# Optimization experiments

Measured on AMD Instinct MI355X. Metric: run time of the kernel, lower is better.

## Reference

```python
import jax, jax.numpy as jnp
import numpy as np

B, T, D, L, H = 8, 1024, 768, 8, 12
BLOCK_SIZE = 4
HD = D // H


def setup_inputs() -> dict:
    key = jax.random.key(0)
    ks = jax.random.split(key, 10)
    sd = 0.02
    return {
        "x_init": jax.random.normal(ks[0], (B, T, D), jnp.float32),
        "attn_proj_w": jax.random.normal(ks[1], (L, D), jnp.float32) * sd,
        "mlp_proj_w": jax.random.normal(ks[2], (L, D), jnp.float32) * sd,
        "Wqkv": jax.random.normal(ks[3], (L, D, 3 * D), jnp.float32) * sd,
        "Wo": jax.random.normal(ks[4], (L, D, D), jnp.float32) * sd,
        "Wm1": jax.random.normal(ks[5], (L, D, 4 * D), jnp.float32) * sd,
        "Wm2": jax.random.normal(ks[6], (L, 4 * D, D), jnp.float32) * sd,
        "attn_scale": 1.0 + jax.random.normal(ks[7], (L, D), jnp.float32) * sd,
        "mlp_scale": 1.0 + jax.random.normal(ks[8], (L, D), jnp.float32) * sd,
        "ln_s": jnp.ones((L,), jnp.float32),
    }


def _rms_norm(x):
    # F.rms_norm with eps=None -> eps = finfo(dtype).eps
    eps = jnp.finfo(x.dtype).eps
    return x * jax.lax.rsqrt(jnp.mean(x * x, axis=-1, keepdims=True) + eps)


def _aggregate(V, q):
    # V: [n, B, T, D]; scalar-query depth attention (keys RMS-normed, values raw)
    K = _rms_norm(V)
    logits = jnp.einsum('d,nbtd->nbt', q, K)
    w = jax.nn.softmax(logits, axis=0)
    return jnp.einsum('nbt,nbtd->btd', w, V)


def _mha(x, wqkv, wo):
    # causal multi-head self-attention
    b, t, d = x.shape
    qkv = x @ wqkv                                   # [b, t, 3D]
    q, k, v = jnp.split(qkv, 3, axis=-1)
    q = q.reshape(b, t, H, HD)
    k = k.reshape(b, t, H, HD)
    v = v.reshape(b, t, H, HD)
    scores = jnp.einsum('bqhd,bkhd->bhqk', q, k) / np.sqrt(HD).astype(np.float32)
    mask = jnp.tril(jnp.ones((t, t), bool))
    scores = jnp.where(mask[None, None], scores, jnp.asarray(-1e30, scores.dtype))
    attn = jax.nn.softmax(scores, axis=-1)
    out = jnp.einsum('bhqk,bkhd->bqhd', attn, v).reshape(b, t, d)
    return out @ wo


def reference(x_init, attn_proj_w, mlp_proj_w, Wqkv, Wo, Wm1, Wm2,
              attn_scale, mlp_scale, ln_s):
    boundary_every = max(1, BLOCK_SIZE // 2)
    hist = [x_init]          # committed block representations
    partial = x_init         # intra-block partial accumulator
    for l in range(L):
        s = ln_s[l]
        V = jnp.stack(hist + [partial], axis=0)          # [n_hist+1, B, T, D]
        h = _aggregate(V, attn_proj_w[l])
        if l % boundary_every == 0:
            hist.append(partial)
            partial = jnp.zeros_like(partial)
        attn_out = _mha(_rms_norm(h) * s, Wqkv[l], Wo[l])
        partial = partial + attn_scale[l][None, None, :] * attn_out
        V2 = jnp.stack(hist + [partial], axis=0)
        h = _aggregate(V2, mlp_proj_w[l])
        mlp_out = jax.nn.gelu((_rms_norm(h) * s) @ Wm1[l]) @ Wm2[l]
        partial = partial + mlp_scale[l][None, None, :] * mlp_out
    return partial
```

## Files before the change

### kernel.cpp

```cpp
#include <hip/hip_runtime.h>
#include <hip/hip_bf16.h>
#include <math.h>
#include <stdint.h>

#define D_MODEL 768
#define T_SEQ   1024
#define B_BATCH 8
#define NHEAD   12
#define HDIM    64
#define NLAYER  8

typedef unsigned short u16;
typedef __attribute__((ext_vector_type(8))) short bf16x8;
typedef __attribute__((ext_vector_type(4))) float f32x4;
typedef __attribute__((ext_vector_type(4))) uint32_t u32x4;

static constexpr size_t BTD  = (size_t)B_BATCH * T_SEQ * D_MODEL;
static constexpr int    ROWS = B_BATCH * T_SEQ;
static constexpr float  EPSF = 1.1920928955078125e-07f;


__device__ __forceinline__ u16 f2bf(float x) {
    __hip_bfloat16 h = __float2bfloat16(x);
    return __builtin_bit_cast(u16, h);
}
__device__ __forceinline__ float bf2f(u16 u) {
    __hip_bfloat16 h = __builtin_bit_cast(__hip_bfloat16, u);
    return __bfloat162float(h);
}
__device__ __forceinline__ void split_bf(float x, u16& hi, u16& lo) {
    hi = f2bf(x);
    lo = f2bf(x - bf2f(hi));
}
__device__ __forceinline__ uint32_t cvt_pk_bf16(float a, float b) {
    uint32_t r;
    asm("v_cvt_pk_bf16_f32 %0, %1, %2" : "=v"(r) : "v"(a), "v"(b));
    return r;
}
__device__ __forceinline__ f32x4 mfma16(bf16x8 a, bf16x8 b, f32x4 c) {
    return __builtin_amdgcn_mfma_f32_16x16x32_bf16(a, b, c, 0, 0, 0);
}

__device__ __forceinline__ void gl_lds16(const void* g, void* l) {
    auto gp = reinterpret_cast<const __attribute__((address_space(1))) char*>(
        reinterpret_cast<uintptr_t>(g));
    auto lp = reinterpret_cast<__attribute__((address_space(3))) char*>(
        static_cast<uint32_t>(reinterpret_cast<uintptr_t>(l)));
    __builtin_amdgcn_global_load_lds(gp, lp, 16, 0, 0);
}

__device__ __forceinline__ float block_reduce_sum(float v, float* sbuf) {
    #pragma unroll
    for (int off = 32; off > 0; off >>= 1) v += __shfl_down(v, off);
    __syncthreads();
    if ((threadIdx.x & 63) == 0) sbuf[threadIdx.x >> 6] = v;
    __syncthreads();
    return sbuf[0] + sbuf[1] + sbuf[2] + sbuf[3];
}

__device__ __forceinline__ float gelu_fast(float x) {
    float z = 0.7978845608028654f * (x + 0.044715f * x * x * x);
    float e = __expf(2.f * z);
    return x - x / (e + 1.f);
}

template<int N>
__global__ __launch_bounds__(256)
void agg_norm_kernel(const float* __restrict__ v0, const float* __restrict__ v1,
                     const float* __restrict__ v2, const float* __restrict__ v3,
                     const float* __restrict__ v4, const float* __restrict__ v5,
                     const float* __restrict__ q,  const float* __restrict__ lns,
                     u16* __restrict__ xh, u16* __restrict__ xl) {
    __shared__ float sbuf[4];
    const float* V[6] = {v0, v1, v2, v3, v4, v5};
    const size_t row = blockIdx.x;
    const int tid = threadIdx.x;

    float qv[3];
    #pragma unroll
    for (int j = 0; j < 3; ++j) qv[j] = q[tid + j * 256];

    float vv[N][3];
    float logits[N];
    #pragma unroll
    for (int i = 0; i < N; ++i) {
        const float* vr = V[i] + row * D_MODEL;
        float ssq = 0.f, qd = 0.f;
        #pragma unroll
        for (int j = 0; j < 3; ++j) {
            float x = vr[tid + j * 256];
            vv[i][j] = x;
            ssq = fmaf(x, x, ssq);
            qd  = fmaf(qv[j], x, qd);
        }
        float S  = block_reduce_sum(ssq, sbuf);
        float Qd = block_reduce_sum(qd,  sbuf);
        logits[i] = Qd * rsqrtf(S * (1.f / 768.f) + EPSF);
    }
    float mx = logits[0];
    #pragma unroll
    for (int i = 1; i < N; ++i) mx = fmaxf(mx, logits[i]);
    float w[N];
    float wsum = 0.f;
    #pragma unroll
    for (int i = 0; i < N; ++i) { w[i] = __expf(logits[i] - mx); wsum += w[i]; }
    float inv = 1.f / wsum;

    float outv[3] = {0.f, 0.f, 0.f};
    #pragma unroll
    for (int i = 0; i < N; ++i) {
        float wi = w[i] * inv;
        #pragma unroll
        for (int j = 0; j < 3; ++j) outv[j] = fmaf(wi, vv[i][j], outv[j]);
    }
    float ssq = 0.f;
    #pragma unroll
    for (int j = 0; j < 3; ++j) ssq = fmaf(outv[j], outv[j], ssq);
    float S2 = block_reduce_sum(ssq, sbuf);
    float scale = lns[0] * rsqrtf(S2 * (1.f / 768.f) + EPSF);
    #pragma unroll
    for (int j = 0; j < 3; ++j) {
        float x = outv[j] * scale;
        u16 hi, lo;
        split_bf(x, hi, lo);
        size_t idx = row * D_MODEL + tid + j * 256;
        xh[idx] = hi;
        xl[idx] = lo;
    }
}

__global__ __launch_bounds__(256)
void transpose_split(const float* __restrict__ W, u16* __restrict__ Th,
                     int K, int N) {
    __shared__ float t[32][33];
    const int bk = blockIdx.x * 32, bn = blockIdx.y * 32;
    const int r = threadIdx.x >> 3, c4 = (threadIdx.x & 7) * 4;
    float4 v = *(const float4*)&W[(size_t)(bk + r) * N + bn + c4];
    t[r][c4 + 0] = v.x; t[r][c4 + 1] = v.y; t[r][c4 + 2] = v.z; t[r][c4 + 3] = v.w;
    __syncthreads();
    u16 h[4];
    #pragma unroll
    for (int j = 0; j < 4; ++j) h[j] = f2bf(t[c4 + j][r]);
    size_t o = (size_t)(bn + r) * K + bk + c4;
    *(uint2*)&Th[o] = make_uint2((uint32_t)h[0] | ((uint32_t)h[1] << 16),
                                 (uint32_t)h[2] | ((uint32_t)h[3] << 16));
}

__global__ __launch_bounds__(256)
void vt_transpose(const u16* __restrict__ vh, u16* __restrict__ vth) {
    __shared__ u16 th[32][36];
    const int bh = blockIdx.z;
    const int t0 = blockIdx.x * 32, d0 = blockIdx.y * 32;
    const int r = threadIdx.x >> 3, c = (threadIdx.x & 7) * 4;
    const size_t ib = ((size_t)(bh << 10) + t0 + r) * 64 + d0 + c;
    *(uint2*)&th[r][c] = *(const uint2*)&vh[ib];
    __syncthreads();
    const size_t ob = ((size_t)(bh << 6) + d0 + r) * 1024 + t0 + c;
    u16 a0 = th[c + 0][r], a1 = th[c + 1][r], a2 = th[c + 2][r], a3 = th[c + 3][r];
    *(uint2*)&vth[ob] = make_uint2((uint32_t)a0 | ((uint32_t)a1 << 16),
                                   (uint32_t)a2 | ((uint32_t)a3 << 16));
}

template<int EPI, int BN, bool TWO>
__global__ __launch_bounds__(256)
void gemm_bf2(const u16* __restrict__ Ah, const u16* __restrict__ Al,
              const u16* __restrict__ Bh,
              float* __restrict__ Cf, u16* __restrict__ Ch,
              const float* __restrict__ scale, int M, int N, int K,
              u16* __restrict__ Qh, u16* __restrict__ Ql,
              u16* __restrict__ Kh, u16* __restrict__ Vh) {
    constexpr int NJ = BN / 32;
    constexpr int A_U16 = TWO ? 8192 : 4096;
    constexpr int BUF_U16 = A_U16 + BN * 32;
    __shared__ u16 smem[2 * BUF_U16];

    const int nwg = gridDim.x * gridDim.y;
    const int lin = blockIdx.y * gridDim.x + blockIdx.x;
    const int wg  = (lin & 7) * (nwg >> 3) + (lin >> 3);
    const int bm  = (wg / gridDim.x) << 7;
    const int bn  = (wg % gridDim.x) * BN;

    const int tid = threadIdx.x;
    const int w = tid >> 6, l = tid & 63;
    const int wr = w >> 1, wc = w & 1;

    const int grow = tid >> 2;
    const int gcol = (((tid & 3) ^ ((tid >> 3) & 3)) << 3);
    const size_t aoff0 = (size_t)(bm + grow) * K + gcol;
    const size_t boff0 = (size_t)(bn + grow) * K + gcol;
    const size_t s64 = (size_t)64 * K;
    char* sb0 = (char*)smem;
    char* sb1 = (char*)smem + 2 * BUF_U16;
    const uint32_t wq = (uint32_t)w << 10;

    auto stage = [&](char* sbuf, int k0) {
        gl_lds16(Ah + aoff0 + k0,       sbuf + 0    + wq);
        gl_lds16(Ah + aoff0 + s64 + k0, sbuf + 4096 + wq);
        if constexpr (TWO) {
            gl_lds16(Al + aoff0 + k0,       sbuf + 8192  + wq);
            gl_lds16(Al + aoff0 + s64 + k0, sbuf + 12288 + wq);
        }
        gl_lds16(Bh + boff0 + k0, sbuf + 2 * A_U16 + wq);
        if constexpr (BN == 128)
            gl_lds16(Bh + boff0 + s64 + k0, sbuf + 2 * A_U16 + 4096 + wq);
    };

    f32x4 acc[4][NJ] = {};

    const int key8 = (((l & 15) >> 1) & 3) << 3;
    const int kswz = ((l >> 4) << 3) ^ key8;
    const int arow = wr * 64 + (l & 15);
    const int brow = wc * (BN / 2) + (l & 15);
    const int nk = K >> 5;

    stage(sb0, 0);
    for (int kt = 0; kt < nk; ++kt) {
        char* cur = (kt & 1) ? sb1 : sb0;
        char* nxt = (kt & 1) ? sb0 : sb1;
        if (kt + 1 < nk) {
            stage(nxt, (kt + 1) << 5);
            if constexpr (TWO && BN == 128)
                asm volatile("s_waitcnt vmcnt(6)\n\ts_barrier" ::: "memory");
            else if constexpr (TWO)
                asm volatile("s_waitcnt vmcnt(5)\n\ts_barrier" ::: "memory");
            else if constexpr (BN == 128)
                asm volatile("s_waitcnt vmcnt(4)\n\ts_barrier" ::: "memory");
            else
                asm volatile("s_waitcnt vmcnt(3)\n\ts_barrier" ::: "memory");
        } else {
            asm volatile("s_waitcnt vmcnt(0)\n\ts_barrier" ::: "memory");
        }
        __builtin_amdgcn_sched_barrier(0);

        const u16* bu = (const u16*)cur;
        bf16x8 ah[4], al4[TWO ? 4 : 1], bh4[NJ];
        #pragma unroll
        for (int i = 0; i < 4; ++i) {
            ah[i] = *(const bf16x8*)&bu[(arow + i * 16) * 32 + kswz];
            if constexpr (TWO)
                al4[i] = *(const bf16x8*)&bu[4096 + (arow + i * 16) * 32 + kswz];
        }
        #pragma unroll
        for (int j = 0; j < NJ; ++j)
            bh4[j] = *(const bf16x8*)&bu[A_U16 + (brow + j * 16) * 32 + kswz];
        asm volatile("s_waitcnt lgkmcnt(0)" ::: "memory");
        __builtin_amdgcn_sched_barrier(0);
        asm volatile("s_barrier" ::: "memory");

        #pragma unroll
        for (int i = 0; i < 4; ++i) {
            #pragma unroll
            for (int j = 0; j < NJ; ++j) {
                acc[i][j] = mfma16(ah[i], bh4[j], acc[i][j]);
                if constexpr (TWO)
                    acc[i][j] = mfma16(al4[i], bh4[j], acc[i][j]);
            }
        }
    }

    const int crow0 = bm + wr * 64 + ((l >> 4) << 2);
    const int ccol0 = bn + wc * (BN / 2) + (l & 15);
    #pragma unroll
    for (int i = 0; i < 4; ++i) {
        #pragma unroll
        for (int j = 0; j < NJ; ++j) {
            const int col = ccol0 + j * 16;
            #pragma unroll
            for (int r = 0; r < 4; ++r) {
                const int row = crow0 + i * 16 + r;
                const size_t o = (size_t)row * N + col;
                float v = acc[i][j][r];
                if (EPI == 1) {
                    Ch[o] = f2bf(gelu_fast(v));
                } else if (EPI == 2) {
                    Cf[o] += scale[col] * v;
                } else if (EPI == 4) {
                    Cf[o] = scale[col] * v;
                } else if (EPI == 3) {
                    const int which = (col >= 1536) ? 2 : ((col >= 768) ? 1 : 0);
                    const int hcol = col - which * 768;
                    const size_t dst = ((size_t)((row >> 10) * NHEAD + (hcol >> 6)) * 1024
                                        + (row & 1023)) * 64 + (hcol & 63);
                    if (which == 0) {
                        v *= 0.125f;
                        u16 hi, lo;
                        split_bf(v, hi, lo);
                        Qh[dst] = hi; Ql[dst] = lo;
                    } else if (which == 1) {
                        Kh[dst] = f2bf(v);
                    } else {
                        Vh[dst] = f2bf(v);
                    }
                }
            }
        }
    }
}

__global__ __launch_bounds__(256, 3)
void flash16(const u16* __restrict__ qh, const u16* __restrict__ ql,
             const u16* __restrict__ kh, const u16* __restrict__ vth,
             u16* __restrict__ ch) {
    const int id = blockIdx.x;
    const int r8 = id & 7, s = id >> 3;
    const int bh = r8 + 8 * (s >> 3);
    const int p  = s & 7;
    const int hh = bh % NHEAD, bb = bh / NHEAD;
    const int tid = threadIdx.x, w = tid >> 6, l = tid & 63;
    const int lq = l & 15, lg = l >> 4;
    const size_t hb = (size_t)bh << 16;

    const int wqA = p * 64 + w * 16;
    const int wqB = (15 - p) * 64 + w * 16;
    const int qA = wqA + lq, qB = wqB + lq;

    bf16x8 qA0, qA1, qA2, qA3, qB0, qB1, qB2, qB3;
    {
        const size_t qa = hb + ((size_t)qA << 6) + lg * 8;
        qA0 = *(const bf16x8*)(qh + qa);       qA1 = *(const bf16x8*)(ql + qa);
        qA2 = *(const bf16x8*)(qh + qa + 32);  qA3 = *(const bf16x8*)(ql + qa + 32);
        const size_t qb = hb + ((size_t)qB << 6) + lg * 8;
        qB0 = *(const bf16x8*)(qh + qb);       qB1 = *(const bf16x8*)(ql + qb);
        qB2 = *(const bf16x8*)(qh + qb + 32);  qB3 = *(const bf16x8*)(ql + qb + 32);
    }

    f32x4 oA[4] = {}, oB[4] = {};
    float mA = -30000.f, lsA = 0.f, mB = -30000.f, lsB = 0.f;
    const int ntiles = 32 - 2 * p;
    const int src0 = 32 * (lg & 1) + lq, src1 = src0 + 16;
    const bool hiHalf = lg >= 2;

    bf16x8 KA[4], KB[4], VA[4], VB[4];
    auto loadK = [&](bf16x8 (&K)[4], int k0) {
        const size_t kb0 = hb + (size_t)(k0 + lq) * 64 + lg * 8;
        const size_t kb1 = kb0 + 16 * 64;
        K[0] = *(const bf16x8*)(kh + kb0);
        K[1] = *(const bf16x8*)(kh + kb0 + 32);
        K[2] = *(const bf16x8*)(kh + kb1);
        K[3] = *(const bf16x8*)(kh + kb1 + 32);
    };
    auto loadV = [&](bf16x8 (&V)[4], int k0) {
        #pragma unroll
        for (int dt = 0; dt < 4; ++dt) {
            const size_t vb = hb + (size_t)(dt * 16 + lq) * 1024 + k0 + lg * 8;
            V[dt] = *(const bf16x8*)(vth + vb);
        }
    };

    auto path = [&](bf16x8 (&Kc)[4], bf16x8 (&vf)[4], int k0, int wqX, int qX,
                    bf16x8 q0, bf16x8 q1, bf16x8 q2, bf16x8 q3,
                    float& mX, float& lsX, f32x4 (&oX)[4]) {
        f32x4 s0 = {}, s1 = {};
        s0 = mfma16(Kc[0], q0, s0); s0 = mfma16(Kc[0], q1, s0);
        s0 = mfma16(Kc[1], q2, s0); s0 = mfma16(Kc[1], q3, s0);
        s1 = mfma16(Kc[2], q0, s1); s1 = mfma16(Kc[2], q1, s1);
        s1 = mfma16(Kc[3], q2, s1); s1 = mfma16(Kc[3], q3, s1);
        if (k0 + 31 > wqX) {
            #pragma unroll
            for (int r = 0; r < 4; ++r) {
                if (k0 + 4 * lg + r > qX)      s0[r] = -30000.f;
                if (k0 + 16 + 4 * lg + r > qX) s1[r] = -30000.f;
            }
        }
        float tmloc = fmaxf(fmaxf(fmaxf(s0[0], s0[1]), fmaxf(s0[2], s0[3])),
                            fmaxf(fmaxf(s1[0], s1[1]), fmaxf(s1[2], s1[3])));
        if (__any(tmloc > mX + 8.f)) {
            float tm = fmaxf(tmloc, __shfl_xor(tmloc, 16));
            tm = fmaxf(tm, __shfl_xor(tm, 32));
            const float mnew = fmaxf(mX, tm);
            const float fac = __expf(mX - mnew);
            mX = mnew;
            lsX *= fac;
            #pragma unroll
            for (int dt = 0; dt < 4; ++dt) {
                oX[dt][0] *= fac; oX[dt][1] *= fac;
                oX[dt][2] *= fac; oX[dt][3] *= fac;
            }
        }
        float ps = 0.f;
        #pragma unroll
        for (int r = 0; r < 4; ++r) {
            s0[r] = __expf(s0[r] - mX); ps += s0[r];
            s1[r] = __expf(s1[r] - mX); ps += s1[r];
        }
        lsX += ps;
        const uint32_t wA0 = cvt_pk_bf16(s0[0], s0[1]);
        const uint32_t wA1 = cvt_pk_bf16(s0[2], s0[3]);
        const uint32_t wB0 = cvt_pk_bf16(s1[0], s1[1]);
        const uint32_t wB1 = cvt_pk_bf16(s1[2], s1[3]);
        const uint32_t a0 = (uint32_t)__shfl((int)wA0, src0);
        const uint32_t b0 = (uint32_t)__shfl((int)wB0, src0);
        const uint32_t a1 = (uint32_t)__shfl((int)wA1, src0);
        const uint32_t b1 = (uint32_t)__shfl((int)wB1, src0);
        const uint32_t a2 = (uint32_t)__shfl((int)wA0, src1);
        const uint32_t b2 = (uint32_t)__shfl((int)wB0, src1);
        const uint32_t a3 = (uint32_t)__shfl((int)wA1, src1);
        const uint32_t b3 = (uint32_t)__shfl((int)wB1, src1);
        u32x4 pw = { hiHalf ? b0 : a0, hiHalf ? b1 : a1,
                     hiHalf ? b2 : a2, hiHalf ? b3 : a3 };
        const bf16x8 pb = __builtin_bit_cast(bf16x8, pw);
        #pragma unroll
        for (int dt = 0; dt < 4; ++dt)
            oX[dt] = mfma16(vf[dt], pb, oX[dt]);
    };

    auto step = [&](bf16x8 (&Kc)[4], bf16x8 (&Vc)[4],
                    bf16x8 (&Kn)[4], bf16x8 (&Vn)[4], int kt) {
        const int k0 = kt * 32;
        const int ktn = (kt + 1 < ntiles) ? kt + 1 : kt;
        loadK(Kn, ktn * 32);
        loadV(Vn, ktn * 32);
        if (k0 <= wqB + 15)
            path(Kc, Vc, k0, wqB, qB, qB0, qB1, qB2, qB3, mB, lsB, oB);
        if (k0 <= wqA + 15)
            path(Kc, Vc, k0, wqA, qA, qA0, qA1, qA2, qA3, mA, lsA, oA);
    };

    loadK(KA, 0);
    loadV(VA, 0);
    for (int kt = 0; kt < ntiles; kt += 2) {
        step(KA, VA, KB, VB, kt);
        step(KB, VB, KA, VA, kt + 1);
    }

    lsA += __shfl_xor(lsA, 16); lsA += __shfl_xor(lsA, 32);
    lsB += __shfl_xor(lsB, 16); lsB += __shfl_xor(lsB, 32);
    const float invA = 1.f / lsA, invB = 1.f / lsB;
    const size_t cbA = ((size_t)(bb * 1024 + qA)) * 768 + hh * 64;
    const size_t cbB = ((size_t)(bb * 1024 + qB)) * 768 + hh * 64;
    #pragma unroll
    for (int dt = 0; dt < 4; ++dt) {
        u16 h4[4];
        #pragma unroll
        for (int r = 0; r < 4; ++r) h4[r] = f2bf(oA[dt][r] * invA);
        size_t co = cbA + dt * 16 + 4 * lg;
        *(uint2*)&ch[co] = make_uint2((uint32_t)h4[0] | ((uint32_t)h4[1] << 16),
                                      (uint32_t)h4[2] | ((uint32_t)h4[3] << 16));
        #pragma unroll
        for (int r = 0; r < 4; ++r) h4[r] = f2bf(oB[dt][r] * invB);
        co = cbB + dt * 16 + 4 * lg;
        *(uint2*)&ch[co] = make_uint2((uint32_t)h4[0] | ((uint32_t)h4[1] << 16),
                                      (uint32_t)h4[2] | ((uint32_t)h4[3] << 16));
    }
}


extern "C" void kernel_launch(void* const* d_in, const int* in_sizes, int n_in,
                              void* d_out, int out_size, void* d_ws, size_t ws_size,
                              hipStream_t stream) {
    const float* x0     = (const float*)d_in[0];
    const float* aproj  = (const float*)d_in[1];
    const float* mproj  = (const float*)d_in[2];
    const float* Wqkv   = (const float*)d_in[3];
    const float* Wo     = (const float*)d_in[4];
    const float* Wm1    = (const float*)d_in[5];
    const float* Wm2    = (const float*)d_in[6];
    const float* ascale = (const float*)d_in[7];
    const float* mscale = (const float*)d_in[8];
    const float* lns    = (const float*)d_in[9];
    float* out = (float*)d_out;
    char*  base = (char*)d_ws;

    float* p1  = (float*)base;
    float* p2  = p1 + BTD;
    float* p3  = p2 + BTD;
    u16*   xnh = (u16*)(base + 12 * BTD);
    u16*   xnl = xnh + BTD;
    u16*   wth = (u16*)(base + 16 * BTD);
    char*  QB  = base + 16 * BTD + (size_t)2 * 3072 * 768;
    u16* qh   = (u16*)QB;
    u16* ql   = qh  + BTD;
    u16* kh   = ql  + BTD;
    u16* vh   = kh  + BTD;
    u16* vth  = vh  + BTD;
    u16* ctxh = vh;
    u16* midh = qh;

    float* pb[3] = {p1, p2, p3};
    const float* hist[6];
    int nh = 1;
    hist[0] = x0;
    const float* partial_c = x0;
    float* partial_w = nullptr;
    int pidx = 0;

    auto launch_agg = [&](int n, const float* Vl6[6], const float* qvec,
                          const float* lnsl) {
        switch (n) {
        case 2: agg_norm_kernel<2><<<dim3(ROWS), 256, 0, stream>>>(Vl6[0], Vl6[1], Vl6[2], Vl6[3], Vl6[4], Vl6[5], qvec, lnsl, xnh, xnl); break;
        case 3: agg_norm_kernel<3><<<dim3(ROWS), 256, 0, stream>>>(Vl6[0], Vl6[1], Vl6[2], Vl6[3], Vl6[4], Vl6[5], qvec, lnsl, xnh, xnl); break;
        case 4: agg_norm_kernel<4><<<dim3(ROWS), 256, 0, stream>>>(Vl6[0], Vl6[1], Vl6[2], Vl6[3], Vl6[4], Vl6[5], qvec, lnsl, xnh, xnl); break;
        case 5: agg_norm_kernel<5><<<dim3(ROWS), 256, 0, stream>>>(Vl6[0], Vl6[1], Vl6[2], Vl6[3], Vl6[4], Vl6[5], qvec, lnsl, xnh, xnl); break;
        default: agg_norm_kernel<6><<<dim3(ROWS), 256, 0, stream>>>(Vl6[0], Vl6[1], Vl6[2], Vl6[3], Vl6[4], Vl6[5], qvec, lnsl, xnh, xnl); break;
        }
    };

    for (int l = 0; l < NLAYER; ++l) {
        const float* Vl6[6] = {nullptr, nullptr, nullptr, nullptr, nullptr, nullptr};
        for (int i = 0; i < nh; ++i) Vl6[i] = hist[i];
        Vl6[nh] = partial_c;
        launch_agg(nh + 1, Vl6, aproj + (size_t)l * D_MODEL, lns + l);

        const bool boundary = ((l & 1) == 0);
        if (boundary) {
            hist[nh++] = partial_c;
            float* np = (pidx < 3) ? pb[pidx] : out;
            ++pidx;
            partial_w = np;
            partial_c = np;
        }

        transpose_split<<<dim3(D_MODEL / 32, 3 * D_MODEL / 32), 256, 0, stream>>>(
            Wqkv + (size_t)l * D_MODEL * 3 * D_MODEL, wth, D_MODEL, 3 * D_MODEL);
        gemm_bf2<3, 128, true><<<dim3(3 * D_MODEL / 128, ROWS / 128), 256, 0, stream>>>(
            xnh, xnl, wth, nullptr, nullptr, nullptr,
            ROWS, 3 * D_MODEL, D_MODEL, qh, ql, kh, vh);

        vt_transpose<<<dim3(T_SEQ / 32, HDIM / 32, B_BATCH * NHEAD), 256, 0, stream>>>(
            vh, vth);

        flash16<<<dim3(768), 256, 0, stream>>>(qh, ql, kh, vth, ctxh);

        transpose_split<<<dim3(D_MODEL / 32, D_MODEL / 32), 256, 0, stream>>>(
            Wo + (size_t)l * D_MODEL * D_MODEL, wth, D_MODEL, D_MODEL);
        if (boundary)
            gemm_bf2<4, 64, false><<<dim3(D_MODEL / 64, ROWS / 128), 256, 0, stream>>>(
                ctxh, nullptr, wth, partial_w, nullptr,
                ascale + (size_t)l * D_MODEL, ROWS, D_MODEL, D_MODEL,
                nullptr, nullptr, nullptr, nullptr);
        else
            gemm_bf2<2, 64, false><<<dim3(D_MODEL / 64, ROWS / 128), 256, 0, stream>>>(
                ctxh, nullptr, wth, partial_w, nullptr,
                ascale + (size_t)l * D_MODEL, ROWS, D_MODEL, D_MODEL,
                nullptr, nullptr, nullptr, nullptr);

        const float* V26[6] = {nullptr, nullptr, nullptr, nullptr, nullptr, nullptr};
        for (int i = 0; i < nh; ++i) V26[i] = hist[i];
        V26[nh] = partial_c;
        launch_agg(nh + 1, V26, mproj + (size_t)l * D_MODEL, lns + l);

        transpose_split<<<dim3(D_MODEL / 32, 4 * D_MODEL / 32), 256, 0, stream>>>(
            Wm1 + (size_t)l * D_MODEL * 4 * D_MODEL, wth, D_MODEL, 4 * D_MODEL);
        gemm_bf2<1, 128, true><<<dim3(4 * D_MODEL / 128, ROWS / 128), 256, 0, stream>>>(
            xnh, xnl, wth, nullptr, midh,
            nullptr, ROWS, 4 * D_MODEL, D_MODEL,
            nullptr, nullptr, nullptr, nullptr);
        transpose_split<<<dim3(4 * D_MODEL / 32, D_MODEL / 32), 256, 0, stream>>>(
            Wm2 + (size_t)l * 4 * D_MODEL * D_MODEL, wth, 4 * D_MODEL, D_MODEL);
        gemm_bf2<2, 64, false><<<dim3(D_MODEL / 64, ROWS / 128), 256, 0, stream>>>(
            midh, nullptr, wth, partial_w, nullptr,
            mscale + (size_t)l * D_MODEL, ROWS, D_MODEL, 4 * D_MODEL,
            nullptr, nullptr, nullptr, nullptr);
    }
}
```

Before: 3.302 ms.

## Drop bf16 hi/lo split for GEMM activations and batch weight transposes per layer

The normalized activations are now stored as a single bf16 value instead of a hi/lo bf16 pair. This halves the A-operand loads and the MFMA count in the QKV and MLP-up GEMMs. The four per-layer weight transpose-and-convert launches are merged into one kernel that writes into separate buffers, which cuts launch count. The cost is lower activation precision in those GEMMs, which may increase error relative to the fp32 reference.

```diff
diff --git a/kernel.cpp b/kernel.cpp
--- a/kernel.cpp
+++ b/kernel.cpp
@@ -70,7 +70,7 @@
                      const float* __restrict__ v2, const float* __restrict__ v3,
                      const float* __restrict__ v4, const float* __restrict__ v5,
                      const float* __restrict__ q,  const float* __restrict__ lns,
-                     u16* __restrict__ xh, u16* __restrict__ xl) {
+                     u16* __restrict__ xh) {
     __shared__ float sbuf[4];
     const float* V[6] = {v0, v1, v2, v3, v4, v5};
     const size_t row = blockIdx.x;
@@ -119,28 +119,32 @@
     float S2 = block_reduce_sum(ssq, sbuf);
     float scale = lns[0] * rsqrtf(S2 * (1.f / 768.f) + EPSF);
     #pragma unroll
-    for (int j = 0; j < 3; ++j) {
-        float x = outv[j] * scale;
-        u16 hi, lo;
-        split_bf(x, hi, lo);
-        size_t idx = row * D_MODEL + tid + j * 256;
-        xh[idx] = hi;
-        xl[idx] = lo;
-    }
+    for (int j = 0; j < 3; ++j)
+        xh[row * D_MODEL + tid + j * 256] = f2bf(outv[j] * scale);
 }
 
 __global__ __launch_bounds__(256)
-void transpose_split(const float* __restrict__ W, u16* __restrict__ Th,
-                     int K, int N) {
-    __shared__ float t[32][33];
-    const int bk = blockIdx.x * 32, bn = blockIdx.y * 32;
+void transpose_all(const float* __restrict__ Wqkv, const float* __restrict__ Wo,
+                   const float* __restrict__ Wm1,  const float* __restrict__ Wm2,
+                   u16* __restrict__ T0, u16* __restrict__ T1,
+                   u16* __restrict__ T2, u16* __restrict__ T3) {
+    const int id = blockIdx.x;
+    const float* W; u16* Th; int K, N, t;
+    if (id < 1728)      { W = Wqkv; Th = T0; K = 768;  N = 2304; t = id; }
+    else if (id < 2304) { W = Wo;   Th = T1; K = 768;  N = 768;  t = id - 1728; }
+    else if (id < 4608) { W = Wm1;  Th = T2; K = 768;  N = 3072; t = id - 2304; }
+    else                { W = Wm2;  Th = T3; K = 3072; N = 768;  t = id - 4608; }
+    const int nk = K >> 5;
+    const int bk = (t % nk) * 32, bn = (t / nk) * 32;
+
+    __shared__ float tt[32][33];
     const int r = threadIdx.x >> 3, c4 = (threadIdx.x & 7) * 4;
     float4 v = *(const float4*)&W[(size_t)(bk + r) * N + bn + c4];
-    t[r][c4 + 0] = v.x; t[r][c4 + 1] = v.y; t[r][c4 + 2] = v.z; t[r][c4 + 3] = v.w;
+    tt[r][c4 + 0] = v.x; tt[r][c4 + 1] = v.y; tt[r][c4 + 2] = v.z; tt[r][c4 + 3] = v.w;
     __syncthreads();
     u16 h[4];
     #pragma unroll
-    for (int j = 0; j < 4; ++j) h[j] = f2bf(t[c4 + j][r]);
+    for (int j = 0; j < 4; ++j) h[j] = f2bf(tt[c4 + j][r]);
     size_t o = (size_t)(bn + r) * K + bk + c4;
     *(uint2*)&Th[o] = make_uint2((uint32_t)h[0] | ((uint32_t)h[1] << 16),
                                  (uint32_t)h[2] | ((uint32_t)h[3] << 16));
@@ -161,17 +165,15 @@
                                    (uint32_t)a2 | ((uint32_t)a3 << 16));
 }
 
-template<int EPI, int BN, bool TWO>
+template<int EPI, int BN>
 __global__ __launch_bounds__(256)
-void gemm_bf2(const u16* __restrict__ Ah, const u16* __restrict__ Al,
-              const u16* __restrict__ Bh,
+void gemm_bf1(const u16* __restrict__ Ah, const u16* __restrict__ Bh,
               float* __restrict__ Cf, u16* __restrict__ Ch,
               const float* __restrict__ scale, int M, int N, int K,
               u16* __restrict__ Qh, u16* __restrict__ Ql,
               u16* __restrict__ Kh, u16* __restrict__ Vh) {
     constexpr int NJ = BN / 32;
-    constexpr int A_U16 = TWO ? 8192 : 4096;
-    constexpr int BUF_U16 = A_U16 + BN * 32;
+    constexpr int BUF_U16 = 4096 + BN * 32;
     __shared__ u16 smem[2 * BUF_U16];
 
     const int nwg = gridDim.x * gridDim.y;
@@ -196,13 +198,9 @@
     auto stage = [&](char* sbuf, int k0) {
         gl_lds16(Ah + aoff0 + k0,       sbuf + 0    + wq);
         gl_lds16(Ah + aoff0 + s64 + k0, sbuf + 4096 + wq);
-        if constexpr (TWO) {
-            gl_lds16(Al + aoff0 + k0,       sbuf + 8192  + wq);
-            gl_lds16(Al + aoff0 + s64 + k0, sbuf + 12288 + wq);
-        }
-        gl_lds16(Bh + boff0 + k0, sbuf + 2 * A_U16 + wq);
+        gl_lds16(Bh + boff0 + k0,       sbuf + 8192 + wq);
         if constexpr (BN == 128)
-            gl_lds16(Bh + boff0 + s64 + k0, sbuf + 2 * A_U16 + 4096 + wq);
+            gl_lds16(Bh + boff0 + s64 + k0, sbuf + 12288 + wq);
     };
 
     f32x4 acc[4][NJ] = {};
@@ -219,11 +217,7 @@
         char* nxt = (kt & 1) ? sb0 : sb1;
         if (kt + 1 < nk) {
             stage(nxt, (kt + 1) << 5);
-            if constexpr (TWO && BN == 128)
-                asm volatile("s_waitcnt vmcnt(6)\n\ts_barrier" ::: "memory");
-            else if constexpr (TWO)
-                asm volatile("s_waitcnt vmcnt(5)\n\ts_barrier" ::: "memory");
-            else if constexpr (BN == 128)
+            if constexpr (BN == 128)
                 asm volatile("s_waitcnt vmcnt(4)\n\ts_barrier" ::: "memory");
             else
                 asm volatile("s_waitcnt vmcnt(3)\n\ts_barrier" ::: "memory");
@@ -233,16 +227,13 @@
         __builtin_amdgcn_sched_barrier(0);
 
         const u16* bu = (const u16*)cur;
-        bf16x8 ah[4], al4[TWO ? 4 : 1], bh4[NJ];
-        #pragma unroll
-        for (int i = 0; i < 4; ++i) {
+        bf16x8 ah[4], bh4[NJ];
+        #pragma unroll
+        for (int i = 0; i < 4; ++i)
             ah[i] = *(const bf16x8*)&bu[(arow + i * 16) * 32 + kswz];
-            if constexpr (TWO)
-                al4[i] = *(const bf16x8*)&bu[4096 + (arow + i * 16) * 32 + kswz];
-        }
         #pragma unroll
         for (int j = 0; j < NJ; ++j)
-            bh4[j] = *(const bf16x8*)&bu[A_U16 + (brow + j * 16) * 32 + kswz];
+            bh4[j] = *(const bf16x8*)&bu[4096 + (brow + j * 16) * 32 + kswz];
         asm volatile("s_waitcnt lgkmcnt(0)" ::: "memory");
         __builtin_amdgcn_sched_barrier(0);
         asm volatile("s_barrier" ::: "memory");
@@ -250,11 +241,8 @@
         #pragma unroll
         for (int i = 0; i < 4; ++i) {
             #pragma unroll
-            for (int j = 0; j < NJ; ++j) {
+            for (int j = 0; j < NJ; ++j)
                 acc[i][j] = mfma16(ah[i], bh4[j], acc[i][j]);
-                if constexpr (TWO)
-                    acc[i][j] = mfma16(al4[i], bh4[j], acc[i][j]);
-            }
         }
     }
 
@@ -465,9 +453,11 @@
     float* p2  = p1 + BTD;
     float* p3  = p2 + BTD;
     u16*   xnh = (u16*)(base + 12 * BTD);
-    u16*   xnl = xnh + BTD;
-    u16*   wth = (u16*)(base + 16 * BTD);
-    char*  QB  = base + 16 * BTD + (size_t)2 * 3072 * 768;
+    u16*   wt0 = (u16*)(base + 14 * BTD);
+    u16*   wt1 = wt0 + (size_t)2304 * 768;
+    u16*   wt2 = wt1 + (size_t)768 * 768;
+    u16*   wt3 = wt2 + (size_t)3072 * 768;
+    char*  QB  = (char*)(wt3 + (size_t)768 * 3072);
     u16* qh   = (u16*)QB;
     u16* ql   = qh  + BTD;
     u16* kh   = ql  + BTD;
@@ -487,15 +477,22 @@
     auto launch_agg = [&](int n, const float* Vl6[6], const float* qvec,
                           const float* lnsl) {
         switch (n) {
-        case 2: agg_norm_kernel<2><<<dim3(ROWS), 256, 0, stream>>>(Vl6[0], Vl6[1], Vl6[2], Vl6[3], Vl6[4], Vl6[5], qvec, lnsl, xnh, xnl); break;
-        case 3: agg_norm_kernel<3><<<dim3(ROWS), 256, 0, stream>>>(Vl6[0], Vl6[1], Vl6[2], Vl6[3], Vl6[4], Vl6[5], qvec, lnsl, xnh, xnl); break;
-        case 4: agg_norm_kernel<4><<<dim3(ROWS), 256, 0, stream>>>(Vl6[0], Vl6[1], Vl6[2], Vl6[3], Vl6[4], Vl6[5], qvec, lnsl, xnh, xnl); break;
-        case 5: agg_norm_kernel<5><<<dim3(ROWS), 256, 0, stream>>>(Vl6[0], Vl6[1], Vl6[2], Vl6[3], Vl6[4], Vl6[5], qvec, lnsl, xnh, xnl); break;
-        default: agg_norm_kernel<6><<<dim3(ROWS), 256, 0, stream>>>(Vl6[0], Vl6[1], Vl6[2], Vl6[3], Vl6[4], Vl6[5], qvec, lnsl, xnh, xnl); break;
+        case 2: agg_norm_kernel<2><<<dim3(ROWS), 256, 0, stream>>>(Vl6[0], Vl6[1], Vl6[2], Vl6[3], Vl6[4], Vl6[5], qvec, lnsl, xnh); break;
+        case 3: agg_norm_kernel<3><<<dim3(ROWS), 256, 0, stream>>>(Vl6[0], Vl6[1], Vl6[2], Vl6[3], Vl6[4], Vl6[5], qvec, lnsl, xnh); break;
+        case 4: agg_norm_kernel<4><<<dim3(ROWS), 256, 0, stream>>>(Vl6[0], Vl6[1], Vl6[2], Vl6[3], Vl6[4], Vl6[5], qvec, lnsl, xnh); break;
+        case 5: agg_norm_kernel<5><<<dim3(ROWS), 256, 0, stream>>>(Vl6[0], Vl6[1], Vl6[2], Vl6[3], Vl6[4], Vl6[5], qvec, lnsl, xnh); break;
+        default: agg_norm_kernel<6><<<dim3(ROWS), 256, 0, stream>>>(Vl6[0], Vl6[1], Vl6[2], Vl6[3], Vl6[4], Vl6[5], qvec, lnsl, xnh); break;
         }
     };
 
     for (int l = 0; l < NLAYER; ++l) {
+        transpose_all<<<dim3(6912), 256, 0, stream>>>(
+            Wqkv + (size_t)l * D_MODEL * 3 * D_MODEL,
+            Wo   + (size_t)l * D_MODEL * D_MODEL,
+            Wm1  + (size_t)l * D_MODEL * 4 * D_MODEL,
+            Wm2  + (size_t)l * 4 * D_MODEL * D_MODEL,
+            wt0, wt1, wt2, wt3);
+
         const float* Vl6[6] = {nullptr, nullptr, nullptr, nullptr, nullptr, nullptr};
         for (int i = 0; i < nh; ++i) Vl6[i] = hist[i];
         Vl6[nh] = partial_c;
@@ -510,10 +507,8 @@
             partial_c = np;
         }
 
-        transpose_split<<<dim3(D_MODEL / 32, 3 * D_MODEL / 32), 256, 0, stream>>>(
-            Wqkv + (size_t)l * D_MODEL * 3 * D_MODEL, wth, D_MODEL, 3 * D_MODEL);
-        gemm_bf2<3, 128, true><<<dim3(3 * D_MODEL / 128, ROWS / 128), 256, 0, stream>>>(
-            xnh, xnl, wth, nullptr, nullptr, nullptr,
+        gemm_bf1<3, 128><<<dim3(3 * D_MODEL / 128, ROWS / 128), 256, 0, stream>>>(
+            xnh, wt0, nullptr, nullptr, nullptr,
             ROWS, 3 * D_MODEL, D_MODEL, qh, ql, kh, vh);
 
         vt_transpose<<<dim3(T_SEQ / 32, HDIM / 32, B_BATCH * NHEAD), 256, 0, stream>>>(
@@ -521,16 +516,14 @@
 
         flash16<<<dim3(768), 256, 0, stream>>>(qh, ql, kh, vth, ctxh);
 
-        transpose_split<<<dim3(D_MODEL / 32, D_MODEL / 32), 256, 0, stream>>>(
-            Wo + (size_t)l * D_MODEL * D_MODEL, wth, D_MODEL, D_MODEL);
         if (boundary)
-            gemm_bf2<4, 64, false><<<dim3(D_MODEL / 64, ROWS / 128), 256, 0, stream>>>(
-                ctxh, nullptr, wth, partial_w, nullptr,
+            gemm_bf1<4, 64><<<dim3(D_MODEL / 64, ROWS / 128), 256, 0, stream>>>(
+                ctxh, wt1, partial_w, nullptr,
                 ascale + (size_t)l * D_MODEL, ROWS, D_MODEL, D_MODEL,
                 nullptr, nullptr, nullptr, nullptr);
         else
-            gemm_bf2<2, 64, false><<<dim3(D_MODEL / 64, ROWS / 128), 256, 0, stream>>>(
-                ctxh, nullptr, wth, partial_w, nullptr,
+            gemm_bf1<2, 64><<<dim3(D_MODEL / 64, ROWS / 128), 256, 0, stream>>>(
+                ctxh, wt1, partial_w, nullptr,
                 ascale + (size_t)l * D_MODEL, ROWS, D_MODEL, D_MODEL,
                 nullptr, nullptr, nullptr, nullptr);
 
@@ -539,16 +532,12 @@
         V26[nh] = partial_c;
         launch_agg(nh + 1, V26, mproj + (size_t)l * D_MODEL, lns + l);
 
-        transpose_split<<<dim3(D_MODEL / 32, 4 * D_MODEL / 32), 256, 0, stream>>>(
-            Wm1 + (size_t)l * D_MODEL * 4 * D_MODEL, wth, D_MODEL, 4 * D_MODEL);
-        gemm_bf2<1, 128, true><<<dim3(4 * D_MODEL / 128, ROWS / 128), 256, 0, stream>>>(
-            xnh, xnl, wth, nullptr, midh,
+        gemm_bf1<1, 128><<<dim3(4 * D_MODEL / 128, ROWS / 128), 256, 0, stream>>>(
+            xnh, wt2, nullptr, midh,
             nullptr, ROWS, 4 * D_MODEL, D_MODEL,
             nullptr, nullptr, nullptr, nullptr);
-        transpose_split<<<dim3(4 * D_MODEL / 32, D_MODEL / 32), 256, 0, stream>>>(
-            Wm2 + (size_t)l * 4 * D_MODEL * D_MODEL, wth, 4 * D_MODEL, D_MODEL);
-        gemm_bf2<2, 64, false><<<dim3(D_MODEL / 64, ROWS / 128), 256, 0, stream>>>(
-            midh, nullptr, wth, partial_w, nullptr,
+        gemm_bf1<2, 64><<<dim3(D_MODEL / 64, ROWS / 128), 256, 0, stream>>>(
+            midh, wt3, partial_w, nullptr,
             mscale + (size_t)l * D_MODEL, ROWS, D_MODEL, 4 * D_MODEL,
             nullptr, nullptr, nullptr, nullptr);
     }
```

Measured after the change: 2.862 ms. 13.3% less time.
